# Kernel tuning notes

Measured on AMD Instinct MI355X. Metric: run time of the kernel, lower is better.

The kernel has to match this reference:

```python
import jax, jax.numpy as jnp
import numpy as np


def _safe_norm(d):
    # Euclidean norm over last axis with torch-style subgradient 0 at 0
    sq = jnp.sum(d * d, axis=-1)
    pos = sq > 0
    return jnp.where(pos, jnp.sqrt(jnp.where(pos, sq, 1.0)), 0.0)


def setup_inputs() -> dict:
    key = jax.random.key(0)
    k1, k2 = jax.random.split(key)
    B, n = 8, 256
    src = jax.random.uniform(k1, (B, n, 2), dtype=jnp.float32) * 2.0 - 1.0
    dst = jax.random.uniform(k2, (B, n, 2), dtype=jnp.float32) * 2.0 - 1.0
    return {"src": src, "dst": dst, "s": 256}


def reference(src, dst, s):
    B, n, _ = src.shape
    dt = src.dtype
    # evaluation grid, matching torch.meshgrid(indexing='ij') then stack((ix,iy))
    lin = jnp.linspace(-1.0, 1.0, s, dtype=dt)
    iy, ix = jnp.meshgrid(lin, lin, indexing="ij")
    gs = jnp.stack((ix, iy), axis=2).reshape(1, -1, 2)  # (1, s*s, 2)

    # TPS system: L wv = rhs
    delta = src[:, :, None, :] - src[:, None, :, :]          # (B,n,n,2)
    K = _safe_norm(delta)                                     # (B,n,n)
    P = jnp.concatenate([jnp.ones((B, n, 1), dt), src], 2)    # (B,n,3)
    top = jnp.concatenate([K, P], 2)                          # (B,n,n+3)
    bot = jnp.concatenate([jnp.swapaxes(P, 1, 2),
                           jnp.zeros((B, 3, 3), dt)], 2)      # (B,3,n+3)
    L = jnp.concatenate([top, bot], 1)                        # (B,n+3,n+3)
    rhs = jnp.concatenate([dst, jnp.zeros((B, 3, 2), dt)], 1) # (B,n+3,2)
    wv = jnp.linalg.solve(L, rhs)                             # (B,n+3,2)

    # evaluate warp on the grid
    S = s * s
    dg = gs[:, :, None, :] - src[:, None, :, :]               # (B,S,n,2)
    Kg = _safe_norm(dg)                                       # (B,S,n)
    gsb = jnp.broadcast_to(gs, (B, S, 2))
    Pg = jnp.concatenate([jnp.ones((B, S, 1), dt), gsb], 2)   # (B,S,3)
    Lg = jnp.concatenate([Kg, Pg], 2)                         # (B,S,n+3)
    out = jnp.matmul(Lg, wv)                                  # (B,S,2)
    return out.reshape(B, s, s, 2).transpose(0, 3, 1, 2)
```

## Files before the change

kernel.cpp:

```cpp
#include <hip/hip_runtime.h>
#include <math.h>

#define NCTRL 256
#define NA    259
#define NAUG  261
#define APITCH 264
#define BATCH 8
#define SGRID 256
#define NB    32
#define NPAN  9
#define PPITCH 36

__global__ __launch_bounds__(256) void build_kernel(const float* __restrict__ src,
                                                    const float* __restrict__ dst,
                                                    float* __restrict__ A){
  const int b = blockIdx.x / 13;
  const int s = blockIdx.x - b*13;
  const int r0 = s*20;
  const int r1 = (r0 + 20 < NA) ? r0 + 20 : NA;
  const float* sb = src + b*NCTRL*2;
  const float* db = dst + b*NCTRL*2;
  float* Ab = A + (size_t)b*NA*APITCH;
  __shared__ float sx[NCTRL], sy[NCTRL];
  {
    int t = threadIdx.x;
    float2 v = ((const float2*)sb)[t];
    sx[t] = v.x; sy[t] = v.y;
  }
  __syncthreads();
  const int total = (r1 - r0)*APITCH;
  for (int idx = threadIdx.x; idx < total; idx += 256){
    int r = r0 + idx / APITCH;
    int c = idx % APITCH;
    float v = 0.0f;
    if (r < NCTRL){
      if (c < NCTRL){
        float dx = sx[r] - sx[c];
        float dy = sy[r] - sy[c];
        v = sqrtf(fmaf(dx, dx, dy*dy));
      } else if (c == NCTRL)   v = 1.0f;
      else if (c == NCTRL+1)   v = sx[r];
      else if (c == NCTRL+2)   v = sy[r];
      else if (c == NA)        v = db[2*r];
      else if (c == NA+1)      v = db[2*r+1];
    } else if (c < NCTRL){
      v = (r == NCTRL) ? 1.0f : ((r == NCTRL+1) ? sx[c] : sy[c]);
    }
    Ab[(size_t)r*APITCH + c] = v;
  }
}

template<int NBC, int NW>
__device__ __forceinline__ void panel_ministeps(
    float (&rr)[NBC], int& org, const int rows,
    const int tid, const int lane, const int wid,
    float (*redrow)[NW][PPITCH], float (*jrow)[PPITCH],
    float (*redv)[NW], int (*redi)[NW], int (*redo_)[NW], int* jorg)
{
  #pragma unroll
  for (int j = 0; j < NBC; ++j){
    const int par = j & 1;
    float bv = (tid >= j && tid < rows) ? fabsf(rr[j]) : -1.0f;
    int bi = tid;
    #pragma unroll
    for (int off = 32; off; off >>= 1){
      float ov = __shfl_xor(bv, off);
      int   oi = __shfl_xor(bi, off);
      if (ov > bv || (ov == bv && oi < bi)){ bv = ov; bi = oi; }
    }
    if (tid == bi){
      redv[par][wid] = bv; redi[par][wid] = bi; redo_[par][wid] = org;
      if (bv >= 0.0f){
        if (NBC == NB){
          #pragma unroll
          for (int q = 0; q < 8; ++q){
            float4 v; v.x=rr[4*q]; v.y=rr[4*q+1]; v.z=rr[4*q+2]; v.w=rr[4*q+3];
            *(float4*)&redrow[par][wid][4*q] = v;
          }
        } else {
          #pragma unroll
          for (int c = 0; c < NBC; ++c) redrow[par][wid][c] = rr[c];
        }
      }
    }
    if (tid == j){
      jorg[par] = org;
      if (NBC == NB){
        #pragma unroll
        for (int q = 0; q < 8; ++q){
          float4 v; v.x=rr[4*q]; v.y=rr[4*q+1]; v.z=rr[4*q+2]; v.w=rr[4*q+3];
          *(float4*)&jrow[par][4*q] = v;
        }
      } else {
        #pragma unroll
        for (int c = 0; c < NBC; ++c) jrow[par][c] = rr[c];
      }
    }
    __syncthreads();
    float gv = redv[par][0]; int gw = 0;
    #pragma unroll
    for (int w = 1; w < NW; ++w){
      if (redv[par][w] > gv ||
          (redv[par][w] == gv && redi[par][w] < redi[par][gw])){
        gv = redv[par][w]; gw = w;
      }
    }
    const int gbi  = redi[par][gw];
    const int gorg = redo_[par][gw];
    float pr[NBC];
    if (NBC == NB){
      #pragma unroll
      for (int q = 0; q < 8; ++q){
        float4 v = *(const float4*)&redrow[par][gw][4*q];
        pr[4*q]=v.x; pr[4*q+1]=v.y; pr[4*q+2]=v.z; pr[4*q+3]=v.w;
      }
    } else {
      #pragma unroll
      for (int c = 0; c < NBC; ++c) pr[c] = redrow[par][gw][c];
    }
    if (gbi != j){
      if (tid == j){
        #pragma unroll
        for (int c = 0; c < NBC; ++c) rr[c] = pr[c];
        org = gorg;
      } else if (tid == gbi){
        #pragma unroll
        for (int c = 0; c < NBC; ++c) rr[c] = jrow[par][c];
        org = jorg[par];
      }
    }
    if (tid > j && tid < rows){
      const float rpiv = 1.0f / pr[j];
      float f = rr[j] * rpiv;
      rr[j] = f;
      #pragma unroll
      for (int c = j+1; c < NBC; ++c) rr[c] = fmaf(-f, pr[c], rr[c]);
    }
  }
}

template<int NBC>
__global__ __launch_bounds__(320) void panel_kernel(float* __restrict__ A,
                                                    int* __restrict__ permbuf,
                                                    int k0, int pidx){
  const int b = blockIdx.x;
  float* Ab = A + (size_t)b*NA*APITCH;
  const int tid  = threadIdx.x;
  const int lane = tid & 63;
  const int wid  = tid >> 6;
  const int rows = NA - k0;

  __shared__ float pan[NA][PPITCH];
  __shared__ float redrow[2][5][PPITCH];
  __shared__ float jrow[2][PPITCH];
  __shared__ float redv[2][5];
  __shared__ int   redi[2][5], redo_[2][5];
  __shared__ int   jorg[2];

  for (int idx = tid; idx < rows*8; idx += 320){
    int i = idx >> 3, q = idx & 7;
    *(float4*)&pan[i][4*q] =
      *(const float4*)(Ab + (size_t)(k0+i)*APITCH + k0 + 4*q);
  }
  __syncthreads();

  float rr[NBC];
  int org = tid;
  if (tid < rows){
    #pragma unroll
    for (int q = 0; q < 8; ++q){
      float4 v = *(const float4*)&pan[tid][4*q];
      rr[4*q]=v.x; rr[4*q+1]=v.y; rr[4*q+2]=v.z; rr[4*q+3]=v.w;
    }
  } else {
    #pragma unroll
    for (int c = 0; c < NBC; ++c) rr[c] = 0.0f;
  }

  panel_ministeps<NBC,5>(rr, org, rows, tid, lane, wid,
                         redrow, jrow, redv, redi, redo_, jorg);

  if (tid < rows){
    #pragma unroll
    for (int q = 0; q < 8; ++q){
      float4 v; v.x=rr[4*q]; v.y=rr[4*q+1]; v.z=rr[4*q+2]; v.w=rr[4*q+3];
      *(float4*)&pan[tid][4*q] = v;
    }
    permbuf[b*(NPAN*NA) + pidx*NA + tid] = org;
  }
  __syncthreads();
  for (int idx = tid; idx < rows*8; idx += 320){
    int i = idx >> 3, q = idx & 7;
    *(float4*)(Ab + (size_t)(k0+i)*APITCH + k0 + 4*q) = *(const float4*)&pan[i][4*q];
  }
}

template<int NBC, int NBCN, bool LOOK>
__global__ __launch_bounds__(256) void update_kernel(float* __restrict__ A,
                                                     int* __restrict__ permbuf,
                                                     int k0, int pidx, int sb){
  const int rows = NA - k0;
  const int ctop = k0 + NBC;
  const int tc   = NAUG - ctop;
  const int b    = blockIdx.x / sb;
  const int s    = blockIdx.x - b*sb;
  const int c0   = s*32;
  const int W    = (tc - c0 < 32) ? (tc - c0) : 32;
  float* Ab = A + (size_t)b*NA*APITCH;
  const int tid  = threadIdx.x;
  const int lane = tid & 63;
  const int wid  = tid >> 6;

  __shared__ float pan[NA][PPITCH];
  __shared__ float stage[NA][PPITCH];
  __shared__ float ustg[NB][PPITCH];
  __shared__ int   perm[NA];
  __shared__ float redrowL[2][4][PPITCH];
  __shared__ float jrowL[2][PPITCH];
  __shared__ float redvL[2][4];
  __shared__ int   rediL[2][4], redoL[2][4];
  __shared__ int   jorgL[2];

  for (int i = tid; i < rows; i += 256)
    perm[i] = permbuf[b*(NPAN*NA) + pidx*NA + i];
  if (NBC == NB){
    for (int idx = tid; idx < rows*8; idx += 256){
      int i = idx >> 3, q = idx & 7;
      *(float4*)&pan[i][4*q] =
        *(const float4*)(Ab + (size_t)(k0+i)*APITCH + k0 + 4*q);
    }
  } else {
    for (int idx = tid; idx < rows*NBC; idx += 256){
      int i = idx / NBC, c = idx - i*NBC;
      pan[i][c] = Ab[(size_t)(k0+i)*APITCH + k0 + c];
    }
  }
  __syncthreads();

  for (int idx = tid; idx < rows*W; idx += 256){
    int i = idx / W, c = idx - i*W;
    stage[i][c] = Ab[(size_t)(k0+perm[i])*APITCH + ctop + c0 + c];
  }
  __syncthreads();

  if (tid < W){
    float u[NBC];
    #pragma unroll
    for (int m = 0; m < NBC; ++m) u[m] = stage[m][tid];
    #pragma unroll
    for (int m = 0; m < NBC; ++m){
      #pragma unroll
      for (int jj = m+1; jj < NBC; ++jj)
        u[jj] = fmaf(-pan[jj][m], u[m], u[jj]);
    }
    #pragma unroll
    for (int m = 0; m < NBC; ++m){
      ustg[m][tid] = u[m];
      Ab[(size_t)(k0+m)*APITCH + ctop + c0 + tid] = u[m];
    }
  }
  __syncthreads();

  const int R = rows - NBC;
  if (R > 0){
    const int rt = (R + 3) >> 2, ct = (W + 3) >> 2;
    for (int t = tid; t < rt*ct; t += 256){
      int tr = t / ct, tcc = t - tr*ct;
      int i0 = tr*4, cc0 = tcc*4;
      const bool full = (cc0 + 4 <= W);
      int ir[4];
      #pragma unroll
      for (int r = 0; r < 4; ++r){
        int i = i0 + r;
        ir[r] = (i < R) ? i : (R - 1);
      }
      float acc[4][4];
      #pragma unroll
      for (int r = 0; r < 4; ++r){
        if (full){
          float4 v = *(const float4*)&stage[NBC + ir[r]][cc0];
          acc[r][0]=v.x; acc[r][1]=v.y; acc[r][2]=v.z; acc[r][3]=v.w;
        } else {
          #pragma unroll
          for (int c = 0; c < 4; ++c)
            acc[r][c] = (cc0 + c < W) ? stage[NBC + ir[r]][cc0 + c] : 0.0f;
        }
      }
      if (NBC == NB){
        #pragma unroll
        for (int mq = 0; mq < NBC/4; ++mq){
          float4 lv[4];
          #pragma unroll
          for (int r = 0; r < 4; ++r)
            lv[r] = *(const float4*)&pan[NBC + ir[r]][4*mq];
          #pragma unroll
          for (int mi = 0; mi < 4; ++mi){
            float4 uv = *(const float4*)&ustg[4*mq + mi][cc0];
            #pragma unroll
            for (int r = 0; r < 4; ++r){
              float l = (mi==0) ? lv[r].x : (mi==1) ? lv[r].y : (mi==2) ? lv[r].z : lv[r].w;
              acc[r][0] = fmaf(-l, uv.x, acc[r][0]);
              acc[r][1] = fmaf(-l, uv.y, acc[r][1]);
              acc[r][2] = fmaf(-l, uv.z, acc[r][2]);
              acc[r][3] = fmaf(-l, uv.w, acc[r][3]);
            }
          }
        }
      } else {
        #pragma unroll
        for (int mi = 0; mi < NBC; ++mi){
          #pragma unroll
          for (int r = 0; r < 4; ++r){
            float l = pan[NBC + ir[r]][mi];
            #pragma unroll
            for (int c = 0; c < 4; ++c)
              acc[r][c] = fmaf(-l, ustg[mi][cc0 + c], acc[r][c]);
          }
        }
      }
      #pragma unroll
      for (int r = 0; r < 4; ++r){
        if (i0 + r < R){
          float* g = Ab + (size_t)(k0 + NBC + i0 + r)*APITCH + ctop + c0 + cc0;
          if (full){
            float4 v; v.x=acc[r][0]; v.y=acc[r][1]; v.z=acc[r][2]; v.w=acc[r][3];
            *(float4*)g = v;
            if (LOOK && s == 0) *(float4*)&stage[NBC + i0 + r][cc0] = v;
          } else {
            #pragma unroll
            for (int c = 0; c < 4; ++c)
              if (cc0 + c < W){
                g[c] = acc[r][c];
                if (LOOK && s == 0) stage[NBC + i0 + r][cc0 + c] = acc[r][c];
              }
          }
        }
      }
    }
  }

  if (LOOK && s == 0){
    __syncthreads();
    const int k0n   = k0 + NBC;
    const int rowsN = rows - NBC;
    float rr[NBCN];
    int org = tid;
    if (tid < rowsN){
      #pragma unroll
      for (int c = 0; c < NBCN; ++c) rr[c] = stage[NBC + tid][c];
    } else {
      #pragma unroll
      for (int c = 0; c < NBCN; ++c) rr[c] = 0.0f;
    }
    panel_ministeps<NBCN,4>(rr, org, rowsN, tid, lane, wid,
                            redrowL, jrowL, redvL, rediL, redoL, jorgL);
    if (tid < rowsN){
      #pragma unroll
      for (int c = 0; c < NBCN; ++c) stage[NBC + tid][c] = rr[c];
      permbuf[b*(NPAN*NA) + (pidx+1)*NA + tid] = org;
    }
    __syncthreads();
    if (NBCN == NB){
      for (int idx = tid; idx < rowsN*8; idx += 256){
        int i = idx >> 3, q = idx & 7;
        *(float4*)(Ab + (size_t)(k0n+i)*APITCH + k0n + 4*q) =
          *(const float4*)&stage[NBC + i][4*q];
      }
    } else {
      for (int idx = tid; idx < rowsN*NBCN; idx += 256){
        int i = idx / NBCN, c = idx - i*NBCN;
        Ab[(size_t)(k0n+i)*APITCH + k0n + c] = stage[NBC + i][c];
      }
    }
  }
}

__global__ __launch_bounds__(512) void backsub_kernel(const float* __restrict__ A,
                                                      float* __restrict__ wv){
  const int b = blockIdx.x;
  const float* Ab = A + (size_t)b*NA*APITCH;
  const int tid  = threadIdx.x;
  const int lane = tid & 63;
  const int wid  = tid >> 6;

  __shared__ float t2[NA][2];
  __shared__ float xs[NA][2];
  __shared__ float u11[NB][NB+1];

  for (int i = tid; i < NA; i += 512){
    t2[i][0] = Ab[(size_t)i*APITCH + NA];
    t2[i][1] = Ab[(size_t)i*APITCH + NA + 1];
  }
  __syncthreads();

  for (int bp = NPAN-1; bp >= 0; --bp){
    const int k0 = bp*NB;
    const int nb = (NA - k0 < NB) ? (NA - k0) : NB;

    for (int idx = tid; idx < nb*nb; idx += 512){
      int r = idx / nb, c = idx - r*nb;
      u11[r][c] = Ab[(size_t)(k0+r)*APITCH + k0 + c];
    }
    __syncthreads();

    if (wid == 0){
      int j = lane >> 1, ch = lane & 1;
      float tval = (j < nb) ? t2[k0+j][ch] : 0.0f;
      for (int k = nb-1; k >= 0; --k){
        float tk = __shfl(tval, 2*k + ch);
        float xk = tk / u11[k][k];
        if (j <  k) tval = fmaf(-u11[j][k], xk, tval);
        if (j == k) tval = xk;
      }
      if (j < nb) xs[k0+j][ch] = tval;
    }
    __syncthreads();

    if (nb == NB){
      const int q = tid & 7;
      for (int base = 0; base < k0; base += 64){
        const int i = base + (tid >> 3);
        float px = 0.0f, py = 0.0f;
        if (i < k0){
          float4 v = *(const float4*)(Ab + (size_t)i*APITCH + k0 + 4*q);
          px = v.x*xs[k0+4*q+0][0] + v.y*xs[k0+4*q+1][0]
             + v.z*xs[k0+4*q+2][0] + v.w*xs[k0+4*q+3][0];
          py = v.x*xs[k0+4*q+0][1] + v.y*xs[k0+4*q+1][1]
             + v.z*xs[k0+4*q+2][1] + v.w*xs[k0+4*q+3][1];
        }
        px += __shfl_xor(px, 1); px += __shfl_xor(px, 2); px += __shfl_xor(px, 4);
        py += __shfl_xor(py, 1); py += __shfl_xor(py, 2); py += __shfl_xor(py, 4);
        if (q == 0 && i < k0){
          t2[i][0] -= px;
          t2[i][1] -= py;
        }
      }
    } else {
      for (int i = tid; i < k0; i += 512){
        float s0 = 0.0f, s1 = 0.0f;
        #pragma unroll
        for (int m = 0; m < 3; ++m){
          float u = Ab[(size_t)i*APITCH + k0 + m];
          s0 = fmaf(u, xs[k0+m][0], s0);
          s1 = fmaf(u, xs[k0+m][1], s1);
        }
        t2[i][0] -= s0;
        t2[i][1] -= s1;
      }
    }
    __syncthreads();
  }

  for (int i = tid; i < NA; i += 512){
    wv[((size_t)b*NA + i)*2 + 0] = xs[i][0];
    wv[((size_t)b*NA + i)*2 + 1] = xs[i][1];
  }
}

__global__ __launch_bounds__(256) void eval_kernel(const float* __restrict__ src,
                                                   const float* __restrict__ wv,
                                                   float* __restrict__ out){
  const int b  = blockIdx.x >> 8;
  const int yi = blockIdx.x & 255;
  const int xi = threadIdx.x;
  __shared__ float2 sxy[NCTRL], wxy[NCTRL];
  const float* sb = src + b*NCTRL*2;
  const float* wb = wv + (size_t)b*NA*2;
  sxy[xi] = ((const float2*)sb)[xi];
  wxy[xi] = ((const float2*)wb)[xi];
  __syncthreads();

  const float step = 2.0f/255.0f;
  const float gx = -1.0f + step*(float)xi;
  const float gy = -1.0f + step*(float)yi;

  float accx = wb[512] + wb[514]*gx + wb[516]*gy;
  float accy = wb[513] + wb[515]*gx + wb[517]*gy;

  #pragma unroll 8
  for (int j = 0; j < NCTRL; ++j){
    float2 s = sxy[j];
    float2 w = wxy[j];
    float dx = gx - s.x;
    float dy = gy - s.y;
    float r = sqrtf(fmaf(dx, dx, dy*dy));
    accx = fmaf(r, w.x, accx);
    accy = fmaf(r, w.y, accy);
  }
  out[((size_t)(b*2    )*SGRID + yi)*SGRID + xi] = accx;
  out[((size_t)(b*2 + 1)*SGRID + yi)*SGRID + xi] = accy;
}

extern "C" void kernel_launch(void* const* d_in, const int* in_sizes, int n_in,
                              void* d_out, int out_size, void* d_ws, size_t ws_size,
                              hipStream_t stream) {
  const float* src = (const float*)d_in[0];
  const float* dst = (const float*)d_in[1];
  float* out = (float*)d_out;

  const size_t matElems = (size_t)BATCH*NA*APITCH;
  float* A     = (float*)d_ws;
  float* wv    = A + matElems;
  int*   permb = (int*)(wv + (size_t)BATCH*NA*2);

  build_kernel<<<BATCH*13, 256, 0, stream>>>(src, dst, A);

  panel_kernel<NB><<<BATCH, 320, 0, stream>>>(A, permb, 0, 0);

  for (int p = 0; p <= 6; ++p){
    const int k0 = p*NB;
    const int tc = NAUG - (k0 + NB);
    const int sb = (tc + 31) >> 5;
    update_kernel<NB, NB, true><<<BATCH*sb, 256, 0, stream>>>(A, permb, k0, p, sb);
  }
  update_kernel<NB, 3, true><<<BATCH, 256, 0, stream>>>(A, permb, 7*NB, 7, 1);
  update_kernel<3, 3, false><<<BATCH, 256, 0, stream>>>(A, permb, 8*NB, 8, 1);

  backsub_kernel<<<BATCH, 512, 0, stream>>>(A, wv);
  eval_kernel<<<BATCH*SGRID, 256, 0, stream>>>(src, wv, out);
}
```

Baseline: 595.4 us.

## Fuse build, LU panels, updates and backsub into one cooperative kernel; tile eval rows

Replaces the chain of build, panel, per-step update and backsubstitution launches with a single cooperative-groups kernel that uses grid.sync between LU steps. This removes about a dozen kernel launch gaps. The eval kernel now computes four grid rows per thread, reusing each control point's dx and packing source and weight into one float4, and uses the hardware sqrt builtin. The cost is grid-wide barriers, 64 fixed blocks that sit partly idle in later steps, and heavier shared memory use per block.

```diff
diff --git a/kernel.cpp b/kernel.cpp
--- a/kernel.cpp
+++ b/kernel.cpp
@@ -1,5 +1,8 @@
 #include <hip/hip_runtime.h>
+#include <hip/hip_cooperative_groups.h>
 #include <math.h>
+
+namespace cg = cooperative_groups;
 
 #define NCTRL 256
 #define NA    259
@@ -10,45 +13,8 @@
 #define NB    32
 #define NPAN  9
 #define PPITCH 36
-
-__global__ __launch_bounds__(256) void build_kernel(const float* __restrict__ src,
-                                                    const float* __restrict__ dst,
-                                                    float* __restrict__ A){
-  const int b = blockIdx.x / 13;
-  const int s = blockIdx.x - b*13;
-  const int r0 = s*20;
-  const int r1 = (r0 + 20 < NA) ? r0 + 20 : NA;
-  const float* sb = src + b*NCTRL*2;
-  const float* db = dst + b*NCTRL*2;
-  float* Ab = A + (size_t)b*NA*APITCH;
-  __shared__ float sx[NCTRL], sy[NCTRL];
-  {
-    int t = threadIdx.x;
-    float2 v = ((const float2*)sb)[t];
-    sx[t] = v.x; sy[t] = v.y;
-  }
-  __syncthreads();
-  const int total = (r1 - r0)*APITCH;
-  for (int idx = threadIdx.x; idx < total; idx += 256){
-    int r = r0 + idx / APITCH;
-    int c = idx % APITCH;
-    float v = 0.0f;
-    if (r < NCTRL){
-      if (c < NCTRL){
-        float dx = sx[r] - sx[c];
-        float dy = sy[r] - sy[c];
-        v = sqrtf(fmaf(dx, dx, dy*dy));
-      } else if (c == NCTRL)   v = 1.0f;
-      else if (c == NCTRL+1)   v = sx[r];
-      else if (c == NCTRL+2)   v = sy[r];
-      else if (c == NA)        v = db[2*r];
-      else if (c == NA+1)      v = db[2*r+1];
-    } else if (c < NCTRL){
-      v = (r == NCTRL) ? 1.0f : ((r == NCTRL+1) ? sx[c] : sy[c]);
-    }
-    Ab[(size_t)r*APITCH + c] = v;
-  }
-}
+#define NT    320
+#define PY    4
 
 template<int NBC, int NW>
 __device__ __forceinline__ void panel_ministeps(
@@ -139,105 +105,42 @@
   }
 }
 
-template<int NBC>
-__global__ __launch_bounds__(320) void panel_kernel(float* __restrict__ A,
-                                                    int* __restrict__ permbuf,
-                                                    int k0, int pidx){
-  const int b = blockIdx.x;
-  float* Ab = A + (size_t)b*NA*APITCH;
-  const int tid  = threadIdx.x;
-  const int lane = tid & 63;
-  const int wid  = tid >> 6;
-  const int rows = NA - k0;
-
-  __shared__ float pan[NA][PPITCH];
-  __shared__ float redrow[2][5][PPITCH];
-  __shared__ float jrow[2][PPITCH];
-  __shared__ float redv[2][5];
-  __shared__ int   redi[2][5], redo_[2][5];
-  __shared__ int   jorg[2];
-
-  for (int idx = tid; idx < rows*8; idx += 320){
-    int i = idx >> 3, q = idx & 7;
-    *(float4*)&pan[i][4*q] =
-      *(const float4*)(Ab + (size_t)(k0+i)*APITCH + k0 + 4*q);
-  }
-  __syncthreads();
-
-  float rr[NBC];
-  int org = tid;
-  if (tid < rows){
-    #pragma unroll
-    for (int q = 0; q < 8; ++q){
-      float4 v = *(const float4*)&pan[tid][4*q];
-      rr[4*q]=v.x; rr[4*q+1]=v.y; rr[4*q+2]=v.z; rr[4*q+3]=v.w;
-    }
-  } else {
-    #pragma unroll
-    for (int c = 0; c < NBC; ++c) rr[c] = 0.0f;
-  }
-
-  panel_ministeps<NBC,5>(rr, org, rows, tid, lane, wid,
-                         redrow, jrow, redv, redi, redo_, jorg);
-
-  if (tid < rows){
-    #pragma unroll
-    for (int q = 0; q < 8; ++q){
-      float4 v; v.x=rr[4*q]; v.y=rr[4*q+1]; v.z=rr[4*q+2]; v.w=rr[4*q+3];
-      *(float4*)&pan[tid][4*q] = v;
-    }
-    permbuf[b*(NPAN*NA) + pidx*NA + tid] = org;
-  }
-  __syncthreads();
-  for (int idx = tid; idx < rows*8; idx += 320){
-    int i = idx >> 3, q = idx & 7;
-    *(float4*)(Ab + (size_t)(k0+i)*APITCH + k0 + 4*q) = *(const float4*)&pan[i][4*q];
-  }
-}
-
 template<int NBC, int NBCN, bool LOOK>
-__global__ __launch_bounds__(256) void update_kernel(float* __restrict__ A,
-                                                     int* __restrict__ permbuf,
-                                                     int k0, int pidx, int sb){
+__device__ __forceinline__ void do_update(
+    float* __restrict__ Ab, int* __restrict__ permbuf,
+    const int b, const int s, const int p,
+    const int tid, const int lane, const int wid,
+    float (*pan)[PPITCH], float (*stage)[PPITCH], float (*ustg)[PPITCH],
+    int* perm,
+    float (*redrow)[5][PPITCH], float (*jrow)[PPITCH],
+    float (*redv)[5], int (*redi)[5], int (*redo_)[5], int* jorg)
+{
+  const int k0   = p*NB;
   const int rows = NA - k0;
   const int ctop = k0 + NBC;
   const int tc   = NAUG - ctop;
-  const int b    = blockIdx.x / sb;
-  const int s    = blockIdx.x - b*sb;
+  const int sbp  = (tc + 31) >> 5;
+  if (s >= sbp) return;
   const int c0   = s*32;
   const int W    = (tc - c0 < 32) ? (tc - c0) : 32;
-  float* Ab = A + (size_t)b*NA*APITCH;
-  const int tid  = threadIdx.x;
-  const int lane = tid & 63;
-  const int wid  = tid >> 6;
-
-  __shared__ float pan[NA][PPITCH];
-  __shared__ float stage[NA][PPITCH];
-  __shared__ float ustg[NB][PPITCH];
-  __shared__ int   perm[NA];
-  __shared__ float redrowL[2][4][PPITCH];
-  __shared__ float jrowL[2][PPITCH];
-  __shared__ float redvL[2][4];
-  __shared__ int   rediL[2][4], redoL[2][4];
-  __shared__ int   jorgL[2];
-
-  for (int i = tid; i < rows; i += 256)
-    perm[i] = permbuf[b*(NPAN*NA) + pidx*NA + i];
+
+  for (int i = tid; i < rows; i += NT)
+    perm[i] = permbuf[b*(NPAN*NA) + p*NA + i];
   if (NBC == NB){
-    for (int idx = tid; idx < rows*8; idx += 256){
+    for (int idx = tid; idx < rows*8; idx += NT){
       int i = idx >> 3, q = idx & 7;
       *(float4*)&pan[i][4*q] =
         *(const float4*)(Ab + (size_t)(k0+i)*APITCH + k0 + 4*q);
     }
   } else {
-    for (int idx = tid; idx < rows*NBC; idx += 256){
+    for (int idx = tid; idx < rows*NBC; idx += NT){
       int i = idx / NBC, c = idx - i*NBC;
       pan[i][c] = Ab[(size_t)(k0+i)*APITCH + k0 + c];
     }
   }
   __syncthreads();
 
-  for (int idx = tid; idx < rows*W; idx += 256){
+  for (int idx = tid; idx < rows*W; idx += NT){
     int i = idx / W, c = idx - i*W;
     stage[i][c] = Ab[(size_t)(k0+perm[i])*APITCH + ctop + c0 + c];
   }
@@ -264,7 +167,7 @@
   const int R = rows - NBC;
   if (R > 0){
     const int rt = (R + 3) >> 2, ct = (W + 3) >> 2;
-    for (int t = tid; t < rt*ct; t += 256){
+    for (int t = tid; t < rt*ct; t += NT){
       int tr = t / ct, tcc = t - tr*ct;
       int i0 = tr*4, cc0 = tcc*4;
       const bool full = (cc0 + 4 <= W);
@@ -352,22 +255,22 @@
       #pragma unroll
       for (int c = 0; c < NBCN; ++c) rr[c] = 0.0f;
     }
-    panel_ministeps<NBCN,4>(rr, org, rowsN, tid, lane, wid,
-                            redrowL, jrowL, redvL, rediL, redoL, jorgL);
+    panel_ministeps<NBCN,5>(rr, org, rowsN, tid, lane, wid,
+                            redrow, jrow, redv, redi, redo_, jorg);
     if (tid < rowsN){
       #pragma unroll
       for (int c = 0; c < NBCN; ++c) stage[NBC + tid][c] = rr[c];
-      permbuf[b*(NPAN*NA) + (pidx+1)*NA + tid] = org;
+      permbuf[b*(NPAN*NA) + (p+1)*NA + tid] = org;
     }
     __syncthreads();
     if (NBCN == NB){
-      for (int idx = tid; idx < rowsN*8; idx += 256){
+      for (int idx = tid; idx < rowsN*8; idx += NT){
         int i = idx >> 3, q = idx & 7;
         *(float4*)(Ab + (size_t)(k0n+i)*APITCH + k0n + 4*q) =
           *(const float4*)&stage[NBC + i][4*q];
       }
     } else {
-      for (int idx = tid; idx < rowsN*NBCN; idx += 256){
+      for (int idx = tid; idx < rowsN*NBCN; idx += NT){
         int i = idx / NBCN, c = idx - i*NBCN;
         Ab[(size_t)(k0n+i)*APITCH + k0n + c] = stage[NBC + i][c];
       }
@@ -375,120 +278,233 @@
   }
 }
 
-__global__ __launch_bounds__(512) void backsub_kernel(const float* __restrict__ A,
-                                                      float* __restrict__ wv){
-  const int b = blockIdx.x;
-  const float* Ab = A + (size_t)b*NA*APITCH;
+__global__ __launch_bounds__(NT) void solve_coop(const float* __restrict__ src,
+                                                 const float* __restrict__ dst,
+                                                 float* __restrict__ A,
+                                                 float* __restrict__ wv,
+                                                 int* __restrict__ permbuf){
+  cg::grid_group grid = cg::this_grid();
+  const int b = blockIdx.x >> 3;
+  const int s = blockIdx.x & 7;
   const int tid  = threadIdx.x;
   const int lane = tid & 63;
   const int wid  = tid >> 6;
-
-  __shared__ float t2[NA][2];
-  __shared__ float xs[NA][2];
+  float* Ab = A + (size_t)b*NA*APITCH;
+
+  __shared__ float pan[NA][PPITCH];
+  __shared__ float stage[NA][PPITCH];
+  __shared__ float ustg[NB][PPITCH];
+  __shared__ int   perm[NA];
+  __shared__ float redrow[2][5][PPITCH];
+  __shared__ float jrow[2][PPITCH];
+  __shared__ float redv[2][5];
+  __shared__ int   redi[2][5], redo_[2][5], jorg[2];
+  __shared__ float sx[NCTRL], sy[NCTRL];
+  __shared__ float t2[NA][2], xs[NA][2];
   __shared__ float u11[NB][NB+1];
 
-  for (int i = tid; i < NA; i += 512){
-    t2[i][0] = Ab[(size_t)i*APITCH + NA];
-    t2[i][1] = Ab[(size_t)i*APITCH + NA + 1];
+  if (tid < NCTRL){
+    float2 v = ((const float2*)(src + b*NCTRL*2))[tid];
+    sx[tid] = v.x; sy[tid] = v.y;
   }
   __syncthreads();
-
-  for (int bp = NPAN-1; bp >= 0; --bp){
-    const int k0 = bp*NB;
-    const int nb = (NA - k0 < NB) ? (NA - k0) : NB;
-
-    for (int idx = tid; idx < nb*nb; idx += 512){
-      int r = idx / nb, c = idx - r*nb;
-      u11[r][c] = Ab[(size_t)(k0+r)*APITCH + k0 + c];
+  {
+    const float* db = dst + b*NCTRL*2;
+    const int r0 = s*33;
+    const int r1 = (r0 + 33 < NA) ? r0 + 33 : NA;
+    const int total = (r1 - r0)*APITCH;
+    for (int idx = tid; idx < total; idx += NT){
+      int r = r0 + idx / APITCH;
+      int c = idx % APITCH;
+      float v = 0.0f;
+      if (r < NCTRL){
+        if (c < NCTRL){
+          float dx = sx[r] - sx[c];
+          float dy = sy[r] - sy[c];
+          v = __builtin_amdgcn_sqrtf(fmaf(dx, dx, dy*dy));
+        } else if (c == NCTRL)   v = 1.0f;
+        else if (c == NCTRL+1)   v = sx[r];
+        else if (c == NCTRL+2)   v = sy[r];
+        else if (c == NA)        v = db[2*r];
+        else if (c == NA+1)      v = db[2*r+1];
+      } else if (c < NCTRL){
+        v = (r == NCTRL) ? 1.0f : ((r == NCTRL+1) ? sx[c] : sy[c]);
+      }
+      Ab[(size_t)r*APITCH + c] = v;
+    }
+  }
+  __threadfence();
+  grid.sync();
+
+  if (s == 0){
+    for (int idx = tid; idx < NA*8; idx += NT){
+      int i = idx >> 3, q = idx & 7;
+      *(float4*)&pan[i][4*q] = *(const float4*)(Ab + (size_t)i*APITCH + 4*q);
     }
     __syncthreads();
-
-    if (wid == 0){
-      int j = lane >> 1, ch = lane & 1;
-      float tval = (j < nb) ? t2[k0+j][ch] : 0.0f;
-      for (int k = nb-1; k >= 0; --k){
-        float tk = __shfl(tval, 2*k + ch);
-        float xk = tk / u11[k][k];
-        if (j <  k) tval = fmaf(-u11[j][k], xk, tval);
-        if (j == k) tval = xk;
-      }
-      if (j < nb) xs[k0+j][ch] = tval;
+    float rr[NB];
+    int org = tid;
+    if (tid < NA){
+      #pragma unroll
+      for (int q = 0; q < 8; ++q){
+        float4 v = *(const float4*)&pan[tid][4*q];
+        rr[4*q]=v.x; rr[4*q+1]=v.y; rr[4*q+2]=v.z; rr[4*q+3]=v.w;
+      }
+    } else {
+      #pragma unroll
+      for (int c = 0; c < NB; ++c) rr[c] = 0.0f;
+    }
+    panel_ministeps<NB,5>(rr, org, NA, tid, lane, wid,
+                          redrow, jrow, redv, redi, redo_, jorg);
+    if (tid < NA){
+      #pragma unroll
+      for (int q = 0; q < 8; ++q){
+        float4 v; v.x=rr[4*q]; v.y=rr[4*q+1]; v.z=rr[4*q+2]; v.w=rr[4*q+3];
+        *(float4*)&pan[tid][4*q] = v;
+      }
+      permbuf[b*(NPAN*NA) + tid] = org;
     }
     __syncthreads();
-
-    if (nb == NB){
-      const int q = tid & 7;
-      for (int base = 0; base < k0; base += 64){
-        const int i = base + (tid >> 3);
-        float px = 0.0f, py = 0.0f;
-        if (i < k0){
-          float4 v = *(const float4*)(Ab + (size_t)i*APITCH + k0 + 4*q);
-          px = v.x*xs[k0+4*q+0][0] + v.y*xs[k0+4*q+1][0]
-             + v.z*xs[k0+4*q+2][0] + v.w*xs[k0+4*q+3][0];
-          py = v.x*xs[k0+4*q+0][1] + v.y*xs[k0+4*q+1][1]
-             + v.z*xs[k0+4*q+2][1] + v.w*xs[k0+4*q+3][1];
-        }
-        px += __shfl_xor(px, 1); px += __shfl_xor(px, 2); px += __shfl_xor(px, 4);
-        py += __shfl_xor(py, 1); py += __shfl_xor(py, 2); py += __shfl_xor(py, 4);
-        if (q == 0 && i < k0){
-          t2[i][0] -= px;
-          t2[i][1] -= py;
-        }
-      }
-    } else {
-      for (int i = tid; i < k0; i += 512){
-        float s0 = 0.0f, s1 = 0.0f;
-        #pragma unroll
-        for (int m = 0; m < 3; ++m){
-          float u = Ab[(size_t)i*APITCH + k0 + m];
-          s0 = fmaf(u, xs[k0+m][0], s0);
-          s1 = fmaf(u, xs[k0+m][1], s1);
-        }
-        t2[i][0] -= s0;
-        t2[i][1] -= s1;
-      }
+    for (int idx = tid; idx < NA*8; idx += NT){
+      int i = idx >> 3, q = idx & 7;
+      *(float4*)(Ab + (size_t)i*APITCH + 4*q) = *(const float4*)&pan[i][4*q];
+    }
+  }
+  __threadfence();
+  grid.sync();
+
+  #pragma unroll 1
+  for (int p = 0; p < 7; ++p){
+    do_update<NB,NB,true>(Ab, permbuf, b, s, p, tid, lane, wid,
+                          pan, stage, ustg, perm, redrow, jrow, redv, redi, redo_, jorg);
+    __threadfence();
+    grid.sync();
+  }
+  do_update<NB,3,true>(Ab, permbuf, b, s, 7, tid, lane, wid,
+                       pan, stage, ustg, perm, redrow, jrow, redv, redi, redo_, jorg);
+  __threadfence();
+  grid.sync();
+  do_update<3,3,false>(Ab, permbuf, b, s, 8, tid, lane, wid,
+                       pan, stage, ustg, perm, redrow, jrow, redv, redi, redo_, jorg);
+  __threadfence();
+  grid.sync();
+
+  if (s == 0){
+    for (int i = tid; i < NA; i += NT){
+      t2[i][0] = Ab[(size_t)i*APITCH + NA];
+      t2[i][1] = Ab[(size_t)i*APITCH + NA + 1];
     }
     __syncthreads();
-  }
-
-  for (int i = tid; i < NA; i += 512){
-    wv[((size_t)b*NA + i)*2 + 0] = xs[i][0];
-    wv[((size_t)b*NA + i)*2 + 1] = xs[i][1];
+    for (int bp = NPAN-1; bp >= 0; --bp){
+      const int k0 = bp*NB;
+      const int nb = (NA - k0 < NB) ? (NA - k0) : NB;
+      for (int idx = tid; idx < nb*nb; idx += NT){
+        int r = idx / nb, c = idx - r*nb;
+        u11[r][c] = Ab[(size_t)(k0+r)*APITCH + k0 + c];
+      }
+      __syncthreads();
+      if (wid == 0){
+        int j = lane >> 1, ch = lane & 1;
+        float tval = (j < nb) ? t2[k0+j][ch] : 0.0f;
+        for (int k = nb-1; k >= 0; --k){
+          float tk = __shfl(tval, 2*k + ch);
+          float xk = tk / u11[k][k];
+          if (j <  k) tval = fmaf(-u11[j][k], xk, tval);
+          if (j == k) tval = xk;
+        }
+        if (j < nb) xs[k0+j][ch] = tval;
+      }
+      __syncthreads();
+      if (nb == NB){
+        const int q = tid & 7;
+        for (int base = 0; base < k0; base += 40){
+          const int i = base + (tid >> 3);
+          float px = 0.0f, py = 0.0f;
+          if (i < k0){
+            float4 v = *(const float4*)(Ab + (size_t)i*APITCH + k0 + 4*q);
+            px = v.x*xs[k0+4*q+0][0] + v.y*xs[k0+4*q+1][0]
+               + v.z*xs[k0+4*q+2][0] + v.w*xs[k0+4*q+3][0];
+            py = v.x*xs[k0+4*q+0][1] + v.y*xs[k0+4*q+1][1]
+               + v.z*xs[k0+4*q+2][1] + v.w*xs[k0+4*q+3][1];
+          }
+          px += __shfl_xor(px, 1); px += __shfl_xor(px, 2); px += __shfl_xor(px, 4);
+          py += __shfl_xor(py, 1); py += __shfl_xor(py, 2); py += __shfl_xor(py, 4);
+          if (q == 0 && i < k0){
+            t2[i][0] -= px;
+            t2[i][1] -= py;
+          }
+        }
+      } else {
+        for (int i = tid; i < k0; i += NT){
+          float s0 = 0.0f, s1 = 0.0f;
+          #pragma unroll
+          for (int m = 0; m < 3; ++m){
+            float u = Ab[(size_t)i*APITCH + k0 + m];
+            s0 = fmaf(u, xs[k0+m][0], s0);
+            s1 = fmaf(u, xs[k0+m][1], s1);
+          }
+          t2[i][0] -= s0;
+          t2[i][1] -= s1;
+        }
+      }
+      __syncthreads();
+    }
+    for (int i = tid; i < NA; i += NT){
+      wv[((size_t)b*NA + i)*2 + 0] = xs[i][0];
+      wv[((size_t)b*NA + i)*2 + 1] = xs[i][1];
+    }
   }
 }
 
 __global__ __launch_bounds__(256) void eval_kernel(const float* __restrict__ src,
                                                    const float* __restrict__ wv,
                                                    float* __restrict__ out){
-  const int b  = blockIdx.x >> 8;
-  const int yi = blockIdx.x & 255;
+  const int b  = blockIdx.x >> 6;
+  const int yg = blockIdx.x & 63;
   const int xi = threadIdx.x;
-  __shared__ float2 sxy[NCTRL], wxy[NCTRL];
+  __shared__ float4 cw[NCTRL];
   const float* sb = src + b*NCTRL*2;
   const float* wb = wv + (size_t)b*NA*2;
-  sxy[xi] = ((const float2*)sb)[xi];
-  wxy[xi] = ((const float2*)wb)[xi];
+  {
+    float2 sv = ((const float2*)sb)[xi];
+    float2 wv2 = ((const float2*)wb)[xi];
+    cw[xi] = make_float4(sv.x, sv.y, wv2.x, wv2.y);
+  }
   __syncthreads();
 
   const float step = 2.0f/255.0f;
   const float gx = -1.0f + step*(float)xi;
-  const float gy = -1.0f + step*(float)yi;
-
-  float accx = wb[512] + wb[514]*gx + wb[516]*gy;
-  float accy = wb[513] + wb[515]*gx + wb[517]*gy;
-
-  #pragma unroll 8
+  const float w0x = wb[512], w1x = wb[514], w2x = wb[516];
+  const float w0y = wb[513], w1y = wb[515], w2y = wb[517];
+
+  float gy[PY], ax[PY], ay[PY];
+  #pragma unroll
+  for (int p = 0; p < PY; ++p){
+    gy[p] = -1.0f + step*(float)(yg*PY + p);
+    ax[p] = w0x + w1x*gx + w2x*gy[p];
+    ay[p] = w0y + w1y*gx + w2y*gy[p];
+  }
+
+  #pragma unroll 4
   for (int j = 0; j < NCTRL; ++j){
-    float2 s = sxy[j];
-    float2 w = wxy[j];
-    float dx = gx - s.x;
-    float dy = gy - s.y;
-    float r = sqrtf(fmaf(dx, dx, dy*dy));
-    accx = fmaf(r, w.x, accx);
-    accy = fmaf(r, w.y, accy);
-  }
-  out[((size_t)(b*2    )*SGRID + yi)*SGRID + xi] = accx;
-  out[((size_t)(b*2 + 1)*SGRID + yi)*SGRID + xi] = accy;
+    float4 c = cw[j];
+    float dx = gx - c.x;
+    float dx2 = dx*dx;
+    #pragma unroll
+    for (int p = 0; p < PY; ++p){
+      float dy = gy[p] - c.y;
+      float r = __builtin_amdgcn_sqrtf(fmaf(dy, dy, dx2));
+      ax[p] = fmaf(r, c.z, ax[p]);
+      ay[p] = fmaf(r, c.w, ay[p]);
+    }
+  }
+
+  const int y0 = yg*PY;
+  #pragma unroll
+  for (int p = 0; p < PY; ++p){
+    out[((size_t)(b*2    )*SGRID + y0 + p)*SGRID + xi] = ax[p];
+    out[((size_t)(b*2 + 1)*SGRID + y0 + p)*SGRID + xi] = ay[p];
+  }
 }
 
 extern "C" void kernel_launch(void* const* d_in, const int* in_sizes, int n_in,
@@ -503,19 +519,9 @@
   float* wv    = A + matElems;
   int*   permb = (int*)(wv + (size_t)BATCH*NA*2);
 
-  build_kernel<<<BATCH*13, 256, 0, stream>>>(src, dst, A);
-
-  panel_kernel<NB><<<BATCH, 320, 0, stream>>>(A, permb, 0, 0);
-
-  for (int p = 0; p <= 6; ++p){
-    const int k0 = p*NB;
-    const int tc = NAUG - (k0 + NB);
-    const int sb = (tc + 31) >> 5;
-    update_kernel<NB, NB, true><<<BATCH*sb, 256, 0, stream>>>(A, permb, k0, p, sb);
-  }
-  update_kernel<NB, 3, true><<<BATCH, 256, 0, stream>>>(A, permb, 7*NB, 7, 1);
-  update_kernel<3, 3, false><<<BATCH, 256, 0, stream>>>(A, permb, 8*NB, 8, 1);
-
-  backsub_kernel<<<BATCH, 512, 0, stream>>>(A, wv);
-  eval_kernel<<<BATCH*SGRID, 256, 0, stream>>>(src, wv, out);
+  void* args[] = {(void*)&src, (void*)&dst, (void*)&A, (void*)&wv, (void*)&permb};
+  hipLaunchCooperativeKernel((void*)solve_coop, dim3(BATCH*8), dim3(NT),
+                             args, 0, stream);
+
+  eval_kernel<<<BATCH*(SGRID/PY), 256, 0, stream>>>(src, wv, out);
 }
```

Result: slower. 798.7 us (+34.1%).
